# Performance work log

Hardware: AMD Instinct MI355X
Metric: run time of the kernel (lower is better)

Reference implementation:

```python
import jax, jax.numpy as jnp
import numpy as np

CD_COEFF = 1.0


def setup_inputs() -> dict:
    key = jax.random.key(0)
    k1, k2 = jax.random.split(key)
    x_diff_pred = jax.random.normal(k1, (16, 2048, 3), dtype=jnp.float32)
    x_diff_target = jax.random.normal(k2, (16, 2048, 3), dtype=jnp.float32)
    return {"x_diff_pred": x_diff_pred, "x_diff_target": x_diff_target}


def _chamfer(p1, p2):
    # p1: (bs, N, 3), p2: (bs, M, 3)
    # squared pairwise distances: (bs, N, M)
    diff = p1[:, :, None, :] - p2[:, None, :, :]
    d2 = jnp.sum(diff * diff, axis=-1)
    # bidirectional min reduction
    min_p1 = jnp.min(d2, axis=2)  # (bs, N): nearest target for each pred point
    min_p2 = jnp.min(d2, axis=1)  # (bs, M): nearest pred for each target point
    return jnp.mean(min_p1) + jnp.mean(min_p2)


def reference(x_diff_pred, x_diff_target):
    cd = _chamfer(x_diff_pred, x_diff_target)
    return CD_COEFF * cd
```

## Files before the change

kernel.cpp:

```cpp
#include <hip/hip_runtime.h>


typedef __attribute__((ext_vector_type(8)))  short s16x8;
typedef __attribute__((ext_vector_type(16))) float f32x16;

#define NPTS   2048
#define BATCH  16
#define MSTRIP 128
#define NSTRIP 16
#define NBLK   256
#define SCALE  (1.0f / 32768.0f)

__device__ __forceinline__ unsigned short bf16_rne(float f) {
    unsigned int u = __float_as_uint(f);
    return (unsigned short)((u + 0x7fffu + ((u >> 16) & 1u)) >> 16);
}
__device__ __forceinline__ float bf16_up(unsigned short h) {
    return __uint_as_float(((unsigned int)h) << 16);
}
__device__ __forceinline__ void split(float v, unsigned short& hi, unsigned short& lo) {
    hi = bf16_rne(v);
    lo = bf16_rne(v - bf16_up(hi));
}

__global__ __launch_bounds__(512) void chamfer_kernel(
    const float* __restrict__ pred,
    const float* __restrict__ tgt,
    float* __restrict__ wscol,
    float* __restrict__ wsrow,
    float* __restrict__ out)
{
    const int bid   = blockIdx.x;
    const int b     = bid >> 4;
    const int strip = bid & 15;
    const int tid   = threadIdx.x;
    const int w  = tid >> 6, l = tid & 63;
    const int cl = l & 31, g = l >> 5, h = w >> 2;

    if (bid == 0 && tid == 0) out[0] = 0.0f;

    const float* Pb = pred + (size_t)b * NPTS * 3;
    const float* Tb = tgt  + (size_t)b * NPTS * 3;

    __shared__ s16x8 bfr[NPTS * 2];
    __shared__ float colpart[4][NPTS];
    __shared__ float rowpart[8][2][16];
    __shared__ float rsum_s[8];

    const unsigned short ONE = 0x3f80;

    {
        const float4* T4 = (const float4*)Tb;
        const float4 va = T4[tid * 3 + 0];
        const float4 vb = T4[tid * 3 + 1];
        const float4 vc = T4[tid * 3 + 2];
        const float xs[4] = {va.x, va.w, vb.z, vc.y};
        const float ys[4] = {va.y, vb.x, vb.w, vc.z};
        const float zs[4] = {va.z, vb.y, vc.x, vc.w};
        #pragma unroll
        for (int k = 0; k < 4; ++k) {
            const int c = tid * 4 + k;
            unsigned short hx, lx, hy, ly, hz, lz, th_, tl_;
            split(xs[k], hx, lx); split(ys[k], hy, ly); split(zs[k], hz, lz);
            const float tt = xs[k]*xs[k] + ys[k]*ys[k] + zs[k]*zs[k];
            split(tt, th_, tl_);
            s16x8 b0, b1;
            b0[0]=(short)hx; b0[1]=(short)hy; b0[2]=(short)hz; b0[3]=(short)hx;
            b0[4]=(short)hy; b0[5]=(short)hz; b0[6]=(short)lx; b0[7]=(short)ly;
            b1[0]=(short)lz; b1[1]=(short)lx; b1[2]=(short)ly; b1[3]=(short)lz;
            b1[4]=(short)ONE; b1[5]=(short)ONE; b1[6]=(short)th_; b1[7]=(short)tl_;
            bfr[(c >> 5) * 64 +      (c & 31)] = b0;
            bfr[(c >> 5) * 64 + 32 + (c & 31)] = b1;
        }
    }

    float rowmin[16];
    #pragma unroll
    for (int r = 0; r < 16; ++r) rowmin[r] = 3.4e38f;

    s16x8 af;
    {
        const int grow = strip * MSTRIP + (w & 3) * 32 + cl;
        const float x = Pb[grow * 3 + 0];
        const float y = Pb[grow * 3 + 1];
        const float z = Pb[grow * 3 + 2];
        const float ax = -2.0f * x, ay = -2.0f * y, az = -2.0f * z;
        const float pp = x * x + y * y + z * z;
        unsigned short phx, plx, phy, ply, phz, plz, pph, ppl;
        split(ax, phx, plx); split(ay, phy, ply); split(az, phz, plz);
        split(pp, pph, ppl);
        s16x8 a0, a1;
        a0[0]=(short)phx; a0[1]=(short)phy; a0[2]=(short)phz; a0[3]=(short)plx;
        a0[4]=(short)ply; a0[5]=(short)plz; a0[6]=(short)phx; a0[7]=(short)phy;
        a1[0]=(short)phz; a1[1]=(short)plx; a1[2]=(short)ply; a1[3]=(short)plz;
        a1[4]=(short)pph; a1[5]=(short)ppl; a1[6]=(short)ONE; a1[7]=(short)ONE;
        af = g ? a1 : a0;
    }

    __syncthreads();

    f32x16 zacc;
    #pragma unroll
    for (int r = 0; r < 16; ++r) zacc[r] = 0.0f;

    #pragma unroll 2
    for (int t = 0; t < 32; ++t) {
        const int gt = h * 32 + t;
        const s16x8 bf = bfr[gt * 64 + l];
        f32x16 acc = __builtin_amdgcn_mfma_f32_32x32x16_bf16(af, bf, zacc, 0, 0, 0);
        #pragma unroll
        for (int r = 0; r < 16; ++r) rowmin[r] = fminf(rowmin[r], acc[r]);
        const float c01 = fminf(acc[0], acc[1]),  c23 = fminf(acc[2], acc[3]);
        const float c45 = fminf(acc[4], acc[5]),  c67 = fminf(acc[6], acc[7]);
        const float c89 = fminf(acc[8], acc[9]),  cab = fminf(acc[10], acc[11]);
        const float ccd = fminf(acc[12], acc[13]), cef = fminf(acc[14], acc[15]);
        float colv = fminf(fminf(fminf(c01, c23), fminf(c45, c67)),
                           fminf(fminf(c89, cab), fminf(ccd, cef)));
        colv = fminf(colv, __shfl_xor(colv, 32));
        colpart[w & 3][gt * 32 + cl] = colv;
    }

    #pragma unroll
    for (int mask = 1; mask < 32; mask <<= 1) {
        #pragma unroll
        for (int r = 0; r < 16; ++r)
            rowmin[r] = fminf(rowmin[r], __shfl_xor(rowmin[r], mask));
    }
    if (cl == 0) {
        #pragma unroll
        for (int r = 0; r < 16; ++r) rowpart[w][g][r] = rowmin[r];
    }
    __syncthreads();

    if (tid < MSTRIP) {
        const int sub = tid >> 5, rr = tid & 31;
        const int gg = (rr >> 2) & 1, reg = (rr & 3) | ((rr >> 3) << 2);
        float v = fminf(rowpart[sub][gg][reg], rowpart[sub + 4][gg][reg]);
        #pragma unroll
        for (int off = 32; off > 0; off >>= 1) v += __shfl_down(v, off);
        if ((tid & 63) == 0) rsum_s[tid >> 6] = v;
    }

    {
        const float4* c0 = (const float4*)colpart[0];
        const float4* c1 = (const float4*)colpart[1];
        const float4* c2 = (const float4*)colpart[2];
        const float4* c3 = (const float4*)colpart[3];
        const float4 v0 = c0[tid], v1 = c1[tid], v2 = c2[tid], v3 = c3[tid];
        float4 o;
        o.x = fminf(fminf(v0.x, v1.x), fminf(v2.x, v3.x));
        o.y = fminf(fminf(v0.y, v1.y), fminf(v2.y, v3.y));
        o.z = fminf(fminf(v0.z, v1.z), fminf(v2.z, v3.z));
        o.w = fminf(fminf(v0.w, v1.w), fminf(v2.w, v3.w));
        ((float4*)(wscol + (size_t)bid * NPTS))[tid] = o;
    }
    __syncthreads();
    if (tid == 0) wsrow[bid] = rsum_s[0] + rsum_s[1];
}

__global__ __launch_bounds__(128) void reduce_kernel(
    const float* __restrict__ wscol,
    const float* __restrict__ wsrow,
    float* __restrict__ out)
{
    const int g    = blockIdx.x;
    const int bb   = g >> 2;
    const int cc   = g & 3;
    const int tid  = threadIdx.x;
    const int lane = tid & 63;
    __shared__ float s2[2];

    const float4* base = (const float4*)(wscol + (size_t)bb * NSTRIP * NPTS
                                               + (size_t)cc * 512);
    float4 m = base[tid];
    #pragma unroll
    for (int s = 1; s < 16; ++s) {
        const float4 v = base[(size_t)s * (NPTS / 4) + tid];
        m.x = fminf(m.x, v.x); m.y = fminf(m.y, v.y);
        m.z = fminf(m.z, v.z); m.w = fminf(m.w, v.w);
    }
    float acc = (m.x + m.y) + (m.z + m.w);

    #pragma unroll
    for (int off = 32; off > 0; off >>= 1)
        acc += __shfl_down(acc, off);
    if (lane == 0) s2[tid >> 6] = acc;
    __syncthreads();

    if (tid == 0) {
        const float rs = (wsrow[4 * g + 0] + wsrow[4 * g + 1])
                       + (wsrow[4 * g + 2] + wsrow[4 * g + 3]);
        atomicAdd(out, ((s2[0] + s2[1]) + rs) * SCALE);
    }
}

extern "C" void kernel_launch(void* const* d_in, const int* in_sizes, int n_in,
                              void* d_out, int out_size, void* d_ws, size_t ws_size,
                              hipStream_t stream)
{
    const float* pred = (const float*)d_in[0];
    const float* tgt  = (const float*)d_in[1];
    float* out   = (float*)d_out;
    float* wscol = (float*)d_ws;
    float* wsrow = (float*)d_ws + (size_t)NBLK * NPTS;

    chamfer_kernel<<<dim3(NBLK), dim3(512), 0, stream>>>(pred, tgt, wscol, wsrow, out);
    reduce_kernel<<<dim3(64), dim3(128), 0, stream>>>(wscol, wsrow, out);
}
```

Baseline: 18.45 us.

## Compute both chamfer directions via separate transposed MFMA passes with fold reductions

Replaces the single MFMA pass, which needed per-row cross-lane shuffle reductions plus a shared column-partial buffer, with two passes. One computes pred×target tiles and folds each accumulator over its 16 values to get per-target column minima. The other computes target×pred tiles (transposed operands) to get per-pred row minima the same way. This drops the 5-level 16-register shuffle tree and the colpart LDS round trip, but doubles the MFMA count, doubles the target-side LDS fragment storage, and adds a launch_bounds occupancy hint.

```diff
diff --git a/kernel.cpp b/kernel.cpp
--- a/kernel.cpp
+++ b/kernel.cpp
@@ -23,7 +23,39 @@
     lo = bf16_rne(v - bf16_up(hi));
 }
 
-__global__ __launch_bounds__(512) void chamfer_kernel(
+#define ONEBF ((short)0x3f80)
+
+__device__ __forceinline__ void mkA(s16x8& a0, s16x8& a1,
+    unsigned short h0, unsigned short h1, unsigned short h2,
+    unsigned short l0, unsigned short l1, unsigned short l2,
+    unsigned short sh, unsigned short sl)
+{
+    a0[0]=(short)h0; a0[1]=(short)h1; a0[2]=(short)h2; a0[3]=(short)l0;
+    a0[4]=(short)l1; a0[5]=(short)l2; a0[6]=(short)h0; a0[7]=(short)h1;
+    a1[0]=(short)h2; a1[1]=(short)l0; a1[2]=(short)l1; a1[3]=(short)l2;
+    a1[4]=(short)sh; a1[5]=(short)sl; a1[6]=ONEBF;     a1[7]=ONEBF;
+}
+__device__ __forceinline__ void mkB(s16x8& b0, s16x8& b1,
+    unsigned short h0, unsigned short h1, unsigned short h2,
+    unsigned short l0, unsigned short l1, unsigned short l2,
+    unsigned short sh, unsigned short sl)
+{
+    b0[0]=(short)h0; b0[1]=(short)h1; b0[2]=(short)h2; b0[3]=(short)h0;
+    b0[4]=(short)h1; b0[5]=(short)h2; b0[6]=(short)l0; b0[7]=(short)l1;
+    b1[0]=(short)l2; b1[1]=(short)l0; b1[2]=(short)l1; b1[3]=(short)l2;
+    b1[4]=ONEBF;     b1[5]=ONEBF;     b1[6]=(short)sh; b1[7]=(short)sl;
+}
+
+__device__ __forceinline__ float fold16(f32x16 a) {
+    const float c0 = fminf(a[0], a[1]),   c1 = fminf(a[2], a[3]);
+    const float c2 = fminf(a[4], a[5]),   c3 = fminf(a[6], a[7]);
+    const float c4 = fminf(a[8], a[9]),   c5 = fminf(a[10], a[11]);
+    const float c6 = fminf(a[12], a[13]), c7 = fminf(a[14], a[15]);
+    return fminf(fminf(fminf(c0, c1), fminf(c2, c3)),
+                 fminf(fminf(c4, c5), fminf(c6, c7)));
+}
+
+__global__ __launch_bounds__(512, 2) void chamfer_kernel(
     const float* __restrict__ pred,
     const float* __restrict__ tgt,
     float* __restrict__ wscol,
@@ -35,19 +67,19 @@
     const int strip = bid & 15;
     const int tid   = threadIdx.x;
     const int w  = tid >> 6, l = tid & 63;
-    const int cl = l & 31, g = l >> 5, h = w >> 2;
+    const int cl = l & 31, g = l >> 5;
 
     if (bid == 0 && tid == 0) out[0] = 0.0f;
 
     const float* Pb = pred + (size_t)b * NPTS * 3;
     const float* Tb = tgt  + (size_t)b * NPTS * 3;
 
-    __shared__ s16x8 bfr[NPTS * 2];
-    __shared__ float colpart[4][NPTS];
-    __shared__ float rowpart[8][2][16];
-    __shared__ float rsum_s[8];
-
-    const unsigned short ONE = 0x3f80;
+    __shared__ s16x8 bfrB[NPTS * 2];
+    __shared__ s16x8 bfrA[NPTS * 2];
+    __shared__ s16x8 pfrA[MSTRIP * 2];
+    __shared__ s16x8 pfrB[MSTRIP * 2];
+    __shared__ float rowpart[8][MSTRIP];
+    __shared__ float rsum_s[2];
 
     {
         const float4* T4 = (const float4*)Tb;
@@ -60,99 +92,110 @@
         #pragma unroll
         for (int k = 0; k < 4; ++k) {
             const int c = tid * 4 + k;
-            unsigned short hx, lx, hy, ly, hz, lz, th_, tl_;
-            split(xs[k], hx, lx); split(ys[k], hy, ly); split(zs[k], hz, lz);
-            const float tt = xs[k]*xs[k] + ys[k]*ys[k] + zs[k]*zs[k];
-            split(tt, th_, tl_);
-            s16x8 b0, b1;
-            b0[0]=(short)hx; b0[1]=(short)hy; b0[2]=(short)hz; b0[3]=(short)hx;
-            b0[4]=(short)hy; b0[5]=(short)hz; b0[6]=(short)lx; b0[7]=(short)ly;
-            b1[0]=(short)lz; b1[1]=(short)lx; b1[2]=(short)ly; b1[3]=(short)lz;
-            b1[4]=(short)ONE; b1[5]=(short)ONE; b1[6]=(short)th_; b1[7]=(short)tl_;
-            bfr[(c >> 5) * 64 +      (c & 31)] = b0;
-            bfr[(c >> 5) * 64 + 32 + (c & 31)] = b1;
+            const float x = xs[k], y = ys[k], z = zs[k];
+            unsigned short hx, lx, hy, ly, hz, lz;
+            unsigned short shx, slx, shy, sly, shz, slz;
+            unsigned short th, tl;
+            split(x, hx, lx); split(y, hy, ly); split(z, hz, lz);
+            split(-2.0f * x, shx, slx); split(-2.0f * y, shy, sly);
+            split(-2.0f * z, shz, slz);
+            split(x * x + y * y + z * z, th, tl);
+            s16x8 b0, b1, a0, a1;
+            mkB(b0, b1, hx, hy, hz, lx, ly, lz, th, tl);
+            mkA(a0, a1, shx, shy, shz, slx, sly, slz, th, tl);
+            const int base = (c >> 5) * 64 + (c & 31);
+            bfrB[base] = b0; bfrB[base + 32] = b1;
+            bfrA[base] = a0; bfrA[base + 32] = a1;
         }
     }
 
-    float rowmin[16];
-    #pragma unroll
-    for (int r = 0; r < 16; ++r) rowmin[r] = 3.4e38f;
-
-    s16x8 af;
-    {
-        const int grow = strip * MSTRIP + (w & 3) * 32 + cl;
+    if (tid < MSTRIP) {
+        const int c = tid;
+        const int grow = strip * MSTRIP + c;
         const float x = Pb[grow * 3 + 0];
         const float y = Pb[grow * 3 + 1];
         const float z = Pb[grow * 3 + 2];
-        const float ax = -2.0f * x, ay = -2.0f * y, az = -2.0f * z;
-        const float pp = x * x + y * y + z * z;
-        unsigned short phx, plx, phy, ply, phz, plz, pph, ppl;
-        split(ax, phx, plx); split(ay, phy, ply); split(az, phz, plz);
-        split(pp, pph, ppl);
-        s16x8 a0, a1;
-        a0[0]=(short)phx; a0[1]=(short)phy; a0[2]=(short)phz; a0[3]=(short)plx;
-        a0[4]=(short)ply; a0[5]=(short)plz; a0[6]=(short)phx; a0[7]=(short)phy;
-        a1[0]=(short)phz; a1[1]=(short)plx; a1[2]=(short)ply; a1[3]=(short)plz;
-        a1[4]=(short)pph; a1[5]=(short)ppl; a1[6]=(short)ONE; a1[7]=(short)ONE;
-        af = g ? a1 : a0;
-    }
-
-    __syncthreads();
+        unsigned short hx, lx, hy, ly, hz, lz;
+        unsigned short shx, slx, shy, sly, shz, slz;
+        unsigned short ph, pl;
+        split(x, hx, lx); split(y, hy, ly); split(z, hz, lz);
+        split(-2.0f * x, shx, slx); split(-2.0f * y, shy, sly);
+        split(-2.0f * z, shz, slz);
+        split(x * x + y * y + z * z, ph, pl);
+        s16x8 a0, a1, b0, b1;
+        mkA(a0, a1, shx, shy, shz, slx, sly, slz, ph, pl);
+        mkB(b0, b1, hx, hy, hz, lx, ly, lz, ph, pl);
+        const int base = (c >> 5) * 64 + (c & 31);
+        pfrA[base] = a0; pfrA[base + 32] = a1;
+        pfrB[base] = b0; pfrB[base + 32] = b1;
+    }
+
+    __syncthreads();
+
+    s16x8 af[4], bp[4];
+    #pragma unroll
+    for (int rt = 0; rt < 4; ++rt) af[rt] = pfrA[rt * 64 + l];
+    #pragma unroll
+    for (int pc = 0; pc < 4; ++pc) bp[pc] = pfrB[pc * 64 + l];
 
     f32x16 zacc;
     #pragma unroll
     for (int r = 0; r < 16; ++r) zacc[r] = 0.0f;
 
+    float tmin[8], pmin[4];
+    #pragma unroll
+    for (int t = 0; t < 8; ++t) tmin[t] = 3.4e38f;
+    #pragma unroll
+    for (int t = 0; t < 4; ++t) pmin[t] = 3.4e38f;
+
     #pragma unroll 2
-    for (int t = 0; t < 32; ++t) {
-        const int gt = h * 32 + t;
-        const s16x8 bf = bfr[gt * 64 + l];
-        f32x16 acc = __builtin_amdgcn_mfma_f32_32x32x16_bf16(af, bf, zacc, 0, 0, 0);
-        #pragma unroll
-        for (int r = 0; r < 16; ++r) rowmin[r] = fminf(rowmin[r], acc[r]);
-        const float c01 = fminf(acc[0], acc[1]),  c23 = fminf(acc[2], acc[3]);
-        const float c45 = fminf(acc[4], acc[5]),  c67 = fminf(acc[6], acc[7]);
-        const float c89 = fminf(acc[8], acc[9]),  cab = fminf(acc[10], acc[11]);
-        const float ccd = fminf(acc[12], acc[13]), cef = fminf(acc[14], acc[15]);
-        float colv = fminf(fminf(fminf(c01, c23), fminf(c45, c67)),
-                           fminf(fminf(c89, cab), fminf(ccd, cef)));
-        colv = fminf(colv, __shfl_xor(colv, 32));
-        colpart[w & 3][gt * 32 + cl] = colv;
-    }
-
-    #pragma unroll
-    for (int mask = 1; mask < 32; mask <<= 1) {
-        #pragma unroll
-        for (int r = 0; r < 16; ++r)
-            rowmin[r] = fminf(rowmin[r], __shfl_xor(rowmin[r], mask));
-    }
-    if (cl == 0) {
-        #pragma unroll
-        for (int r = 0; r < 16; ++r) rowpart[w][g][r] = rowmin[r];
+    for (int ct = 0; ct < 8; ++ct) {
+        const s16x8 bf = bfrB[(w * 8 + ct) * 64 + l];
+        #pragma unroll
+        for (int rt = 0; rt < 4; ++rt) {
+            const f32x16 acc =
+                __builtin_amdgcn_mfma_f32_32x32x16_bf16(af[rt], bf, zacc, 0, 0, 0);
+            tmin[ct] = fminf(tmin[ct], fold16(acc));
+        }
+    }
+
+    #pragma unroll 2
+    for (int rt2 = 0; rt2 < 8; ++rt2) {
+        const s16x8 at = bfrA[(w * 8 + rt2) * 64 + l];
+        #pragma unroll
+        for (int pc = 0; pc < 4; ++pc) {
+            const f32x16 acc =
+                __builtin_amdgcn_mfma_f32_32x32x16_bf16(at, bp[pc], zacc, 0, 0, 0);
+            pmin[pc] = fminf(pmin[pc], fold16(acc));
+        }
+    }
+
+    #pragma unroll
+    for (int ct = 0; ct < 8; ++ct)
+        tmin[ct] = fminf(tmin[ct], __shfl_xor(tmin[ct], 32));
+    #pragma unroll
+    for (int pc = 0; pc < 4; ++pc)
+        pmin[pc] = fminf(pmin[pc], __shfl_xor(pmin[pc], 32));
+
+    if (g == 0) {
+        #pragma unroll
+        for (int ct = 0; ct < 8; ++ct)
+            wscol[(size_t)bid * NPTS + w * 256 + ct * 32 + cl] = tmin[ct];
+        #pragma unroll
+        for (int pc = 0; pc < 4; ++pc)
+            rowpart[w][pc * 32 + cl] = pmin[pc];
     }
     __syncthreads();
 
     if (tid < MSTRIP) {
-        const int sub = tid >> 5, rr = tid & 31;
-        const int gg = (rr >> 2) & 1, reg = (rr & 3) | ((rr >> 3) << 2);
-        float v = fminf(rowpart[sub][gg][reg], rowpart[sub + 4][gg][reg]);
-        #pragma unroll
-        for (int off = 32; off > 0; off >>= 1) v += __shfl_down(v, off);
+        float v = rowpart[0][tid];
+        #pragma unroll
+        for (int ww = 1; ww < 8; ++ww)
+            v = fminf(v, rowpart[ww][tid]);
+        #pragma unroll
+        for (int off = 32; off > 0; off >>= 1)
+            v += __shfl_down(v, off);
         if ((tid & 63) == 0) rsum_s[tid >> 6] = v;
-    }
-
-    {
-        const float4* c0 = (const float4*)colpart[0];
-        const float4* c1 = (const float4*)colpart[1];
-        const float4* c2 = (const float4*)colpart[2];
-        const float4* c3 = (const float4*)colpart[3];
-        const float4 v0 = c0[tid], v1 = c1[tid], v2 = c2[tid], v3 = c3[tid];
-        float4 o;
-        o.x = fminf(fminf(v0.x, v1.x), fminf(v2.x, v3.x));
-        o.y = fminf(fminf(v0.y, v1.y), fminf(v2.y, v3.y));
-        o.z = fminf(fminf(v0.z, v1.z), fminf(v2.z, v3.z));
-        o.w = fminf(fminf(v0.w, v1.w), fminf(v2.w, v3.w));
-        ((float4*)(wscol + (size_t)bid * NPTS))[tid] = o;
     }
     __syncthreads();
     if (tid == 0) wsrow[bid] = rsum_s[0] + rsum_s[1];
```

After: 20.18 us. 1.09x slower.
